# Kernel tuning notes

Hardware: AMD Instinct MI355X
Metric: run time of the kernel (lower is better)

## Reference

```python
import jax, jax.numpy as jnp
import numpy as np

B, D, C, E = 8192, 3072, 512, 8  # batch, img dim, code dim, n_experts


def setup_inputs() -> dict:
    key = jax.random.key(0)
    k1, k2, k3, k4 = jax.random.split(key, 4)
    img = jax.random.normal(k1, (B, D), dtype=jnp.float32)
    label = jax.random.randint(k2, (B,), 0, E, dtype=jnp.int64)
    # per-expert encoder/decoder weights (Linear layers), scaled like torch default init
    W_enc = jax.random.normal(k3, (E, C, D), dtype=jnp.float32) * (1.0 / np.sqrt(D))
    b_enc = jnp.zeros((E, C), dtype=jnp.float32)
    W_dec = jax.random.normal(k4, (E, D, C), dtype=jnp.float32) * (1.0 / np.sqrt(C))
    b_dec = jnp.zeros((E, D), dtype=jnp.float32)
    return {"img": img, "label": label, "W_enc": W_enc, "b_enc": b_enc,
            "W_dec": W_dec, "b_dec": b_dec}


def reference(img, label, W_enc, b_enc, W_dec, b_dec):
    # Label-routed dispatch: each row goes through the encoder/decoder of its
    # label's expert, results scattered back into a full [B, D] tensor.
    # Reference form: loop over the fixed, small expert set and select by mask
    # (identical math to gather -> expert -> scatter in the original).
    decoded = jnp.zeros_like(img)
    for e in range(E):
        code_e = jax.nn.relu(img @ W_enc[e].T + b_enc[e])      # [B, C]
        dec_e = code_e @ W_dec[e].T + b_dec[e]                 # [B, D]
        decoded = jnp.where((label == e)[:, None], dec_e, decoded)
    loss = jnp.mean((decoded - img) ** 2)
    return loss, decoded
```

## Files before the change

### kernel.cpp

```cpp
#include <hip/hip_runtime.h>
#include <hip/hip_bf16.h>

#define B_ 8192
#define D_ 3072
#define C_ 512
#define E_ 8

typedef float  floatx4 __attribute__((ext_vector_type(4)));
typedef __bf16 bf16x8  __attribute__((ext_vector_type(8)));
typedef __bf16 bf16x4  __attribute__((ext_vector_type(4)));

__device__ __forceinline__ bf16x4 cvt4(float4 v) {
    bf16x4 o;
    o[0] = (__bf16)v.x; o[1] = (__bf16)v.y; o[2] = (__bf16)v.z; o[3] = (__bf16)v.w;
    return o;
}

__device__ __forceinline__ void dma16(const void* g, void* l) {
    __builtin_amdgcn_global_load_lds(
        (const __attribute__((address_space(1))) unsigned int*)(uintptr_t)g,
        (__attribute__((address_space(3))) unsigned int*)(uintptr_t)l,
        16, 0, 0);
}

__global__ void k_count(const int* __restrict__ label, int* __restrict__ counts) {
    int b = blockIdx.x * blockDim.x + threadIdx.x;
    if (b < B_) atomicAdd(&counts[label[b]], 1);
}

__global__ void k_offsets(const int* __restrict__ counts, int* __restrict__ offsets) {
    if (threadIdx.x == 0 && blockIdx.x == 0) {
        int s = 0;
        for (int e = 0; e < E_; ++e) { offsets[e] = s; s += counts[e]; }
    }
}

__global__ void k_scatter(const int* __restrict__ label, const int* __restrict__ offsets,
                          int* __restrict__ cursors, int* __restrict__ row_ids) {
    int b = blockIdx.x * blockDim.x + threadIdx.x;
    if (b < B_) {
        int e = label[b];
        int p = atomicAdd(&cursors[e], 1);
        row_ids[offsets[e] + p] = b;
    }
}

#define D4_ (D_ / 4)
#define NI_ (B_ * D4_)
#define NW_ (E_ * C_ * D4_)
__global__ __launch_bounds__(256)
void k_prep(const float4* __restrict__ img4, const int* __restrict__ row_ids,
            const float4* __restrict__ We4, const float4* __restrict__ Wd4,
            bf16x4* __restrict__ imgG4, bf16x4* __restrict__ We16_4,
            bf16x4* __restrict__ Wd16_4)
{
    int i = blockIdx.x * 256 + threadIdx.x;
    const int stride = gridDim.x * 256;
    const int total = NI_ + 2 * NW_;
    for (; i < total; i += stride) {
        if (i < NI_) {
            int row = i / D4_;
            int c   = i - row * D4_;
            float4 v = img4[(size_t)row_ids[row] * D4_ + c];
            imgG4[i] = cvt4(v);
        } else if (i < NI_ + NW_) {
            int j = i - NI_;
            We16_4[j] = cvt4(We4[j]);
        } else {
            int j = i - NI_ - NW_;
            Wd16_4[j] = cvt4(Wd4[j]);
        }
    }
}

__global__ __launch_bounds__(256, 3)
void enc_kernel(const __bf16* __restrict__ imgG, const __bf16* __restrict__ We16,
                const float* __restrict__ benc, const int* __restrict__ counts,
                const int* __restrict__ offsets, __bf16* __restrict__ code)
{
    const int e   = blockIdx.z;
    const int cnt = counts[e];
    const int bid = blockIdx.y * gridDim.x + blockIdx.x;
    const int swz = (bid & 7) * 64 + (bid >> 3);
    const int m0  = (swz & 127) * 64;
    const int n0  = (swz >> 7) * 128;
    if (m0 >= cnt) return;
    const int off = offsets[e];

    __shared__ __align__(16) __bf16 As[4][64][32];
    __shared__ __align__(16) __bf16 Bs[4][128][32];

    const int tid  = threadIdx.x;
    const int lane = tid & 63;
    const int wave = tid >> 6;
    const int wm   = wave >> 1;
    const int wn   = wave & 1;

    const int drow = tid >> 2;
    const int gsw  = (((tid & 3) ^ ((tid >> 3) & 3)) << 3);
    const __bf16* ag0 = imgG + (size_t)(off + m0 + drow) * D_ + gsw;
    const __bf16* bg0 = We16 + ((size_t)e * C_ + n0 + drow) * D_ + gsw;
    const __bf16* bg1 = bg0 + (size_t)64 * D_;
    char* lA = (char*)As + tid * 16;
    char* lB = (char*)Bs + tid * 16;

#define STG(buf, step) do {                                  \
        const size_t ko_ = (size_t)(step) * 32;              \
        dma16(ag0 + ko_, lA + (buf) * 4096);                 \
        dma16(bg0 + ko_, lB + (buf) * 8192);                 \
        dma16(bg1 + ko_, lB + (buf) * 8192 + 4096);          \
    } while (0)

    STG(0, 0);
    STG(1, 1);
    STG(2, 2);

    floatx4 acc[2][4];
    #pragma unroll
    for (int i = 0; i < 2; ++i)
        #pragma unroll
        for (int j = 0; j < 4; ++j)
            acc[i][j] = (floatx4){0.f, 0.f, 0.f, 0.f};

    const int fr = lane & 15;
    const int g4 = lane >> 4;
    const int psw = ((g4 ^ ((fr >> 1) & 3)) << 4);
    const char* Ab = (const char*)As + (wm * 32 + fr) * 64 + psw;
    const char* Bb = (const char*)Bs + (wn * 64 + fr) * 64 + psw;

    const int NS = D_ / 32;
    #pragma unroll 4
    for (int s = 0; s < NS; ++s) {
        asm volatile("s_waitcnt vmcnt(6)" ::: "memory");
        __builtin_amdgcn_s_barrier();
        asm volatile("" ::: "memory");
        __builtin_amdgcn_sched_barrier(0);
        const int ps = (s + 3 < NS) ? (s + 3) : (NS - 1);
        STG((s + 3) & 3, ps);
        const char* pA = Ab + (s & 3) * 4096;
        const char* pB = Bb + (s & 3) * 8192;
        bf16x8 af[2], bq[4];
        #pragma unroll
        for (int i = 0; i < 2; ++i) af[i] = *(const bf16x8*)(pA + i * 1024);
        #pragma unroll
        for (int j = 0; j < 4; ++j) bq[j] = *(const bf16x8*)(pB + j * 1024);
        __builtin_amdgcn_s_setprio(1);
        #pragma unroll
        for (int mt = 0; mt < 2; ++mt)
            #pragma unroll
            for (int nt = 0; nt < 4; ++nt)
                acc[mt][nt] = __builtin_amdgcn_mfma_f32_16x16x32_bf16(af[mt], bq[nt], acc[mt][nt], 0, 0, 0);
        __builtin_amdgcn_s_setprio(0);
    }
#undef STG
    asm volatile("s_waitcnt vmcnt(0)" ::: "memory");

    const int rq = g4 << 2;
    #pragma unroll
    for (int nt = 0; nt < 4; ++nt) {
        const int gcol = n0 + wn * 64 + nt * 16 + fr;
        const float bias = benc[e * C_ + gcol];
        #pragma unroll
        for (int mt = 0; mt < 2; ++mt)
            #pragma unroll
            for (int reg = 0; reg < 4; ++reg) {
                const int g = m0 + wm * 32 + mt * 16 + rq + reg;
                if (g < cnt) {
                    float v = acc[mt][nt][reg] + bias;
                    v = v > 0.f ? v : 0.f;
                    code[(size_t)(off + g) * C_ + gcol] = (__bf16)v;
                }
            }
    }
}

__global__ __launch_bounds__(256, 6)
void dec_kernel(const __bf16* __restrict__ imgG, const __bf16* __restrict__ Wd16,
                const float* __restrict__ bdec, const int* __restrict__ row_ids,
                const int* __restrict__ counts, const int* __restrict__ offsets,
                const __bf16* __restrict__ code, float* __restrict__ decoded,
                double* __restrict__ loss_acc)
{
    const int e   = blockIdx.z;
    const int cnt = counts[e];
    const int bid = blockIdx.y * gridDim.x + blockIdx.x;
    const int swz = (bid & 7) * 384 + (bid >> 3);
    const int m0  = (swz & 63) * 128;
    const int n0  = (swz >> 6) * 64;
    if (m0 >= cnt) return;
    const int off = offsets[e];

    __shared__ __align__(16) __bf16 As[2][128][32];
    __shared__ __align__(16) __bf16 Bs[2][64][32];
    __shared__ float red[4];

    const int tid  = threadIdx.x;
    const int lane = tid & 63;
    const int wave = tid >> 6;
    const int wm   = wave >> 1;
    const int wn   = wave & 1;

    const int drow = tid >> 2;
    const int gsw  = (((tid & 3) ^ ((tid >> 3) & 3)) << 3);
    const __bf16* ag0 = code + (size_t)(off + m0 + drow) * C_ + gsw;
    const __bf16* ag1 = ag0 + (size_t)64 * C_;
    const __bf16* bg0 = Wd16 + ((size_t)e * D_ + n0 + drow) * C_ + gsw;
    char* lA = (char*)As + tid * 16;
    char* lB = (char*)Bs + tid * 16;

#define STG(buf, step) do {                                  \
        const size_t ko_ = (size_t)(step) * 32;              \
        dma16(ag0 + ko_, lA + (buf) * 8192);                 \
        dma16(ag1 + ko_, lA + (buf) * 8192 + 4096);          \
        dma16(bg0 + ko_, lB + (buf) * 4096);                 \
    } while (0)

    STG(0, 0);

    floatx4 acc[4][2];
    #pragma unroll
    for (int i = 0; i < 4; ++i)
        #pragma unroll
        for (int j = 0; j < 2; ++j)
            acc[i][j] = (floatx4){0.f, 0.f, 0.f, 0.f};

    const int fr = lane & 15;
    const int g4 = lane >> 4;
    const int psw = ((g4 ^ ((fr >> 1) & 3)) << 4);
    const char* Ab = (const char*)As + (wm * 64 + fr) * 64 + psw;
    const char* Bb = (const char*)Bs + (wn * 32 + fr) * 64 + psw;

    const int NS = C_ / 32;
    #pragma unroll 4
    for (int s = 0; s < NS; ++s) {
        asm volatile("s_waitcnt vmcnt(0)" ::: "memory");
        __builtin_amdgcn_s_barrier();
        asm volatile("" ::: "memory");
        __builtin_amdgcn_sched_barrier(0);
        if (s + 1 < NS) STG((s + 1) & 1, s + 1);
        const char* pA = Ab + (s & 1) * 8192;
        const char* pB = Bb + (s & 1) * 4096;
        bf16x8 af[4], bq[2];
        #pragma unroll
        for (int i = 0; i < 4; ++i) af[i] = *(const bf16x8*)(pA + i * 1024);
        #pragma unroll
        for (int j = 0; j < 2; ++j) bq[j] = *(const bf16x8*)(pB + j * 1024);
        __builtin_amdgcn_s_setprio(1);
        #pragma unroll
        for (int mt = 0; mt < 4; ++mt)
            #pragma unroll
            for (int nt = 0; nt < 2; ++nt)
                acc[mt][nt] = __builtin_amdgcn_mfma_f32_16x16x32_bf16(af[mt], bq[nt], acc[mt][nt], 0, 0, 0);
        __builtin_amdgcn_s_setprio(0);
    }
#undef STG

    const int rq = g4 << 2;
    int orig[4][4];
    #pragma unroll
    for (int mt = 0; mt < 4; ++mt)
        #pragma unroll
        for (int reg = 0; reg < 4; ++reg) {
            const int g = m0 + wm * 64 + mt * 16 + rq + reg;
            orig[mt][reg] = (g < cnt) ? row_ids[off + g] : -1;
        }

    float lsum = 0.f;
    #pragma unroll
    for (int nt = 0; nt < 2; ++nt) {
        const int gcol = n0 + wn * 32 + nt * 16 + fr;
        const float bias = bdec[e * D_ + gcol];
        #pragma unroll
        for (int mt = 0; mt < 4; ++mt)
            #pragma unroll
            for (int reg = 0; reg < 4; ++reg) {
                if (orig[mt][reg] >= 0) {
                    const int g = m0 + wm * 64 + mt * 16 + rq + reg;
                    float v = acc[mt][nt][reg] + bias;
                    decoded[(size_t)orig[mt][reg] * D_ + gcol] = v;
                    float d = v - (float)imgG[(size_t)(off + g) * D_ + gcol];
                    lsum += d * d;
                }
            }
    }
    #pragma unroll
    for (int o = 32; o > 0; o >>= 1) lsum += __shfl_down(lsum, o, 64);
    if (lane == 0) red[wave] = lsum;
    __syncthreads();
    if (tid == 0) atomicAdd(loss_acc, (double)(red[0] + red[1] + red[2] + red[3]));
}

__global__ void k_final(const double* __restrict__ loss_acc, float* __restrict__ out) {
    if (threadIdx.x == 0 && blockIdx.x == 0)
        out[0] = (float)(*loss_acc / (double)((size_t)B_ * (size_t)D_));
}

extern "C" void kernel_launch(void* const* d_in, const int* in_sizes, int n_in,
                              void* d_out, int out_size, void* d_ws, size_t ws_size,
                              hipStream_t stream)
{
    const float* img   = (const float*)d_in[0];
    const int*   label = (const int*)d_in[1];
    const float* Wenc  = (const float*)d_in[2];
    const float* benc  = (const float*)d_in[3];
    const float* Wdec  = (const float*)d_in[4];
    const float* bdec  = (const float*)d_in[5];
    float* out = (float*)d_out;

    char* ws = (char*)d_ws;
    int*    counts  = (int*)(ws + 0);
    int*    cursors = (int*)(ws + 32);
    int*    offsets = (int*)(ws + 64);
    double* loss    = (double*)(ws + 96);
    int*    row_ids = (int*)(ws + 128);
    __bf16* code = (__bf16*)(ws + 65536);
    __bf16* imgG = (__bf16*)(ws + 65536 + 8519680);
    __bf16* We16 = (__bf16*)(ws + 65536 + 8519680 + 51118080);
    __bf16* Wd16 = (__bf16*)(ws + 65536 + 8519680 + 51118080 + 25165824);

    hipMemsetAsync(d_ws, 0, 128, stream);
    k_count  <<<dim3(B_ / 256), dim3(256), 0, stream>>>(label, counts);
    k_offsets<<<dim3(1),        dim3(64),  0, stream>>>(counts, offsets);
    k_scatter<<<dim3(B_ / 256), dim3(256), 0, stream>>>(label, offsets, cursors, row_ids);
    k_prep   <<<dim3(2048),     dim3(256), 0, stream>>>(
        (const float4*)img, row_ids, (const float4*)Wenc, (const float4*)Wdec,
        (bf16x4*)imgG, (bf16x4*)We16, (bf16x4*)Wd16);
    enc_kernel<<<dim3(C_ / 128, B_ / 64, E_), dim3(256), 0, stream>>>(
        imgG, We16, benc, counts, offsets, code);
    dec_kernel<<<dim3(D_ / 64, B_ / 128, E_), dim3(256), 0, stream>>>(
        imgG, Wd16, bdec, row_ids, counts, offsets, code, out + 1, loss);
    k_final<<<dim3(1), dim3(64), 0, stream>>>(loss, out);
}
```

Measured before the change: 551.4 us.

## Fuse routing kernels and launch encoder over compact per-expert tile list

```diff
diff --git a/kernel.cpp b/kernel.cpp
--- a/kernel.cpp
+++ b/kernel.cpp
@@ -5,6 +5,7 @@
 #define D_ 3072
 #define C_ 512
 #define E_ 8
+#define MAXTILES_ 136
 
 typedef float  floatx4 __attribute__((ext_vector_type(4)));
 typedef __bf16 bf16x8  __attribute__((ext_vector_type(8)));
@@ -23,25 +24,33 @@
         16, 0, 0);
 }
 
-__global__ void k_count(const int* __restrict__ label, int* __restrict__ counts) {
-    int b = blockIdx.x * blockDim.x + threadIdx.x;
-    if (b < B_) atomicAdd(&counts[label[b]], 1);
-}
-
-__global__ void k_offsets(const int* __restrict__ counts, int* __restrict__ offsets) {
-    if (threadIdx.x == 0 && blockIdx.x == 0) {
-        int s = 0;
-        for (int e = 0; e < E_; ++e) { offsets[e] = s; s += counts[e]; }
-    }
-}
-
-__global__ void k_scatter(const int* __restrict__ label, const int* __restrict__ offsets,
-                          int* __restrict__ cursors, int* __restrict__ row_ids) {
-    int b = blockIdx.x * blockDim.x + threadIdx.x;
-    if (b < B_) {
+__global__ __launch_bounds__(1024)
+void k_route(const int* __restrict__ label, int* __restrict__ counts,
+             int* __restrict__ offsets, int* __restrict__ row_ids,
+             int* __restrict__ tile_e, int* __restrict__ tile_m,
+             int* __restrict__ ntiles, double* __restrict__ loss)
+{
+    __shared__ int cnt_s[E_], off_s[E_], cur_s[E_];
+    const int tid = threadIdx.x;
+    if (tid < E_) cnt_s[tid] = 0;
+    __syncthreads();
+    for (int b = tid; b < B_; b += 1024) atomicAdd(&cnt_s[label[b]], 1);
+    __syncthreads();
+    if (tid == 0) {
+        int s = 0, t = 0;
+        for (int e = 0; e < E_; ++e) {
+            off_s[e] = s; offsets[e] = s; counts[e] = cnt_s[e]; cur_s[e] = 0;
+            for (int m = 0; m < cnt_s[e]; m += 64) { tile_e[t] = e; tile_m[t] = m; ++t; }
+            s += cnt_s[e];
+        }
+        *ntiles = t;
+        *loss = 0.0;
+    }
+    __syncthreads();
+    for (int b = tid; b < B_; b += 1024) {
         int e = label[b];
-        int p = atomicAdd(&cursors[e], 1);
-        row_ids[offsets[e] + p] = b;
+        int p = atomicAdd(&cur_s[e], 1);
+        row_ids[off_s[e] + p] = b;
     }
 }
 
@@ -76,15 +85,18 @@
 __global__ __launch_bounds__(256, 3)
 void enc_kernel(const __bf16* __restrict__ imgG, const __bf16* __restrict__ We16,
                 const float* __restrict__ benc, const int* __restrict__ counts,
-                const int* __restrict__ offsets, __bf16* __restrict__ code)
-{
-    const int e   = blockIdx.z;
+                const int* __restrict__ offsets, const int* __restrict__ tile_e,
+                const int* __restrict__ tile_m, const int* __restrict__ ntiles,
+                __bf16* __restrict__ code)
+{
+    const int bid = blockIdx.y * gridDim.x + blockIdx.x;
+    const int swz = (bid & 7) * 68 + (bid >> 3);
+    const int t   = swz % MAXTILES_;
+    const int n0  = (swz / MAXTILES_) * 128;
+    if (t >= *ntiles) return;
+    const int e   = tile_e[t];
+    const int m0  = tile_m[t];
     const int cnt = counts[e];
-    const int bid = blockIdx.y * gridDim.x + blockIdx.x;
-    const int swz = (bid & 7) * 64 + (bid >> 3);
-    const int m0  = (swz & 127) * 64;
-    const int n0  = (swz >> 7) * 128;
-    if (m0 >= cnt) return;
     const int off = offsets[e];
 
     __shared__ __align__(16) __bf16 As[4][64][32];
@@ -309,24 +321,24 @@
 
     char* ws = (char*)d_ws;
     int*    counts  = (int*)(ws + 0);
-    int*    cursors = (int*)(ws + 32);
     int*    offsets = (int*)(ws + 64);
     double* loss    = (double*)(ws + 96);
     int*    row_ids = (int*)(ws + 128);
+    int*    tile_e  = (int*)(ws + 40960);
+    int*    tile_m  = (int*)(ws + 41984);
+    int*    ntiles  = (int*)(ws + 43008);
     __bf16* code = (__bf16*)(ws + 65536);
     __bf16* imgG = (__bf16*)(ws + 65536 + 8519680);
     __bf16* We16 = (__bf16*)(ws + 65536 + 8519680 + 51118080);
     __bf16* Wd16 = (__bf16*)(ws + 65536 + 8519680 + 51118080 + 25165824);
 
-    hipMemsetAsync(d_ws, 0, 128, stream);
-    k_count  <<<dim3(B_ / 256), dim3(256), 0, stream>>>(label, counts);
-    k_offsets<<<dim3(1),        dim3(64),  0, stream>>>(counts, offsets);
-    k_scatter<<<dim3(B_ / 256), dim3(256), 0, stream>>>(label, offsets, cursors, row_ids);
-    k_prep   <<<dim3(2048),     dim3(256), 0, stream>>>(
+    k_route<<<dim3(1), dim3(1024), 0, stream>>>(
+        label, counts, offsets, row_ids, tile_e, tile_m, ntiles, loss);
+    k_prep <<<dim3(2048), dim3(256), 0, stream>>>(
         (const float4*)img, row_ids, (const float4*)Wenc, (const float4*)Wdec,
         (bf16x4*)imgG, (bf16x4*)We16, (bf16x4*)Wd16);
-    enc_kernel<<<dim3(C_ / 128, B_ / 64, E_), dim3(256), 0, stream>>>(
-        imgG, We16, benc, counts, offsets, code);
+    enc_kernel<<<dim3(C_ / 128, MAXTILES_, 1), dim3(256), 0, stream>>>(
+        imgG, We16, benc, counts, offsets, tile_e, tile_m, ntiles, code);
     dec_kernel<<<dim3(D_ / 64, B_ / 128, E_), dim3(256), 0, stream>>>(
         imgG, Wd16, bdec, row_ids, counts, offsets, code, out + 1, loss);
     k_final<<<dim3(1), dim3(64), 0, stream>>>(loss, out);
```

Result: faster. 445.5 us (-19.2%).
